# Kernel optimization log

Measured on AMD Instinct MI355X. Metric: run time of the kernel, lower is better.

## Reference

```python
import jax, jax.numpy as jnp
import numpy as np

NUM_SEGMENTS = 64  # number of bags (max batch id + 1)
TEMP = 1.0
EPS_NORM = 1e-12
EPS_SOFTMAX = 1e-16

D = 1024
L = 128
N = 262144


def setup_inputs() -> dict:
    key = jax.random.key(0)
    ks = jax.random.split(key, 8)
    feature = jax.random.normal(ks[0], (N, D), dtype=jnp.float32)
    batch = jnp.sort(jax.random.randint(ks[1], (N,), 0, NUM_SEGMENTS, dtype=jnp.int32))
    # xavier_normal_ init: std = sqrt(2/(fan_in+fan_out))
    Wa = jax.random.normal(ks[2], (L, D), dtype=jnp.float32) * np.sqrt(2.0 / (D + L))
    ba = jnp.zeros((L,), dtype=jnp.float32)
    Wb = jax.random.normal(ks[3], (L, D), dtype=jnp.float32) * np.sqrt(2.0 / (D + L))
    bb = jnp.zeros((L,), dtype=jnp.float32)
    Wc = jax.random.normal(ks[4], (1, L), dtype=jnp.float32) * np.sqrt(2.0 / (L + 1))
    bc = jnp.zeros((1,), dtype=jnp.float32)
    return {"feature": feature, "batch": batch, "istrain": 0,
            "Wa": Wa, "ba": ba, "Wb": Wb, "bb": bb, "Wc": Wc, "bc": bc}


def segment_softmax(score, batch, num_segments):
    # score: [N, 1], batch: [N] segment ids (torch_geometric softmax semantics)
    seg_max = jax.ops.segment_max(score, batch, num_segments=num_segments)
    ex = jnp.exp(score - seg_max[batch])
    denom = jax.ops.segment_sum(ex, batch, num_segments=num_segments)
    return ex / (denom[batch] + EPS_SOFTMAX)


def reference(feature, batch, istrain, Wa, ba, Wb, bb, Wc, bc):
    # F.normalize: L2-normalize each row (dim=1)
    norm = jnp.linalg.norm(feature, axis=1, keepdims=True)
    instance_norm_feature = feature / jnp.maximum(norm, EPS_NORM)
    a = jax.nn.sigmoid(feature @ Wa.T + ba)          # [N, L]
    b = jnp.tanh(feature @ Wb.T + bb)                # [N, L]
    gated = a * b                                     # [N, L]
    score = (gated @ Wc.T + bc) / TEMP               # [N, 1]
    score = segment_softmax(score, batch, NUM_SEGMENTS)
    # istrain=0 -> dropout is identity in this reference
    return (instance_norm_feature, score)
```

## Files before the change

### kernel.cpp

```cpp
#include <hip/hip_runtime.h>

#define DD 1024
#define LL 128
#define NSEG 64
#define CHS 544
#define GRID 1024
#define NT 16

typedef float floatx4 __attribute__((ext_vector_type(4)));

__global__ __launch_bounds__(256)
void prep_kernel(const float* __restrict__ Wa, const float* __restrict__ Wb,
                 unsigned char* __restrict__ Wf8, float* __restrict__ denom,
                 float* __restrict__ score_raw)
{
    int gid = blockIdx.x * 256 + threadIdx.x;
    if (gid < 2 * LL * DD) {
        const int j    = gid & 7;
        const int lane = (gid >> 3) & 63;
        const int ct   = (gid >> 9) & 15;
        const int c    = gid >> 13;
        const int r = ct * 16 + (lane & 15);
        const int k = c * 32 + (lane >> 4) * 8 + j;
        const float v = ((r < LL) ? Wa[r * DD + k] : Wb[(r - LL) * DD + k]) * 16.0f;
        unsigned u = __builtin_amdgcn_cvt_pk_fp8_f32(v, v, 0, false);
        Wf8[gid] = (unsigned char)(u & 0xFF);
        score_raw[gid] = 0.0f;
    }
    if (gid < NSEG) denom[gid] = 0.0f;
}

__global__ __launch_bounds__(512, 8)
void fused_main(const float* __restrict__ feat,
                const unsigned char* __restrict__ Wf8,
                const float* __restrict__ ba,
                const float* __restrict__ bb,
                const float* __restrict__ Wc,
                float* __restrict__ out_norm,
                float* __restrict__ score_raw)
{
    __shared__ __align__(16) char tile[32 * CHS];

    const int tid  = threadIdx.x;
    const int wave = tid >> 6;
    const int lane = tid & 63;
    const int s15  = lane & 15;
    const int l4   = lane >> 4;
    const int bid  = blockIdx.x;

    const float bav = ba[wave * 16 + s15];
    const float bbv = bb[wave * 16 + s15];
    const float wcv = Wc[wave * 16 + s15];
    const unsigned char* bb0 = Wf8 + (size_t)wave * 512 + (size_t)lane * 8;

    float4 L[2][4];

    auto issue = [&](int T) {
        const float* fb = feat + ((size_t)T * 16 + wave * 2) * DD + lane * 4;
        #pragma unroll
        for (int i = 0; i < 2; ++i)
            #pragma unroll
            for (int c = 0; c < 4; ++c)
                L[i][c] = *reinterpret_cast<const float4*>(fb + (size_t)i * DD + c * 256);
    };

    issue(bid);

    for (int it = 0; it < NT; ++it) {
        const int T = bid + it * GRID;

        unsigned pw[2][4];
        #pragma unroll
        for (int i = 0; i < 2; ++i) {
            float ss = 0.0f;
            #pragma unroll
            for (int c = 0; c < 4; ++c)
                ss += L[i][c].x * L[i][c].x + L[i][c].y * L[i][c].y
                    + L[i][c].z * L[i][c].z + L[i][c].w * L[i][c].w;
            #pragma unroll
            for (int off = 32; off >= 1; off >>= 1) ss += __shfl_xor(ss, off);
            const float rinv = 1.0f / fmaxf(sqrtf(ss), 1e-12f);

            float* ob = out_norm + ((size_t)T * 16 + wave * 2 + i) * DD + lane * 4;
            #pragma unroll
            for (int c = 0; c < 4; ++c) {
                float4 v;
                v.x = L[i][c].x * rinv; v.y = L[i][c].y * rinv;
                v.z = L[i][c].z * rinv; v.w = L[i][c].w * rinv;
                *reinterpret_cast<float4*>(ob + c * 256) = v;
            }
            #pragma unroll
            for (int c = 0; c < 4; ++c) {
                unsigned u = __builtin_amdgcn_cvt_pk_fp8_f32(L[i][c].x * 8.0f, L[i][c].y * 8.0f, 0, false);
                u = __builtin_amdgcn_cvt_pk_fp8_f32(L[i][c].z * 8.0f, L[i][c].w * 8.0f, u, true);
                pw[i][c] = u;
            }
        }

        __syncthreads();
        #pragma unroll
        for (int i = 0; i < 2; ++i) {
            const int r = wave * 2 + i;
            #pragma unroll
            for (int c = 0; c < 4; ++c) {
                const int chunk = (lane >> 3) + c * 8;
                const int addr  = chunk * CHS + r * 32 + ((lane >> 1) & 3) * 8 + (lane & 1) * 4;
                *reinterpret_cast<unsigned*>(tile + addr) = pw[i][c];
            }
        }
        __syncthreads();

        if (it + 1 < NT) issue(T + GRID);
        __builtin_amdgcn_sched_barrier(0);

        floatx4 acc0 = (floatx4)0.0f;
        floatx4 acc1 = (floatx4)0.0f;
        #pragma unroll 2
        for (int c = 0; c < 32; ++c) {
            const long long a8 = *reinterpret_cast<const long long*>(tile + c * CHS + s15 * 32 + l4 * 8);
            const long long w0 = *reinterpret_cast<const long long*>(bb0 + (size_t)c * 8192);
            const long long w1 = *reinterpret_cast<const long long*>(bb0 + (size_t)c * 8192 + 4096);
            acc0 = __builtin_amdgcn_mfma_f32_16x16x32_fp8_fp8(a8, w0, acc0, 0, 0, 0);
            acc1 = __builtin_amdgcn_mfma_f32_16x16x32_fp8_fp8(a8, w1, acc1, 0, 0, 0);
        }

        {
            const float S = 1.0f / 128.0f;
            float s[4];
            #pragma unroll
            for (int j = 0; j < 4; ++j) {
                const float av = 1.0f / (1.0f + expf(-(acc0[j] * S + bav)));
                const float bv = tanhf(acc1[j] * S + bbv);
                s[j] = av * bv * wcv;
            }
            #pragma unroll
            for (int j = 0; j < 4; ++j) {
                s[j] += __shfl_xor(s[j], 1);
                s[j] += __shfl_xor(s[j], 2);
                s[j] += __shfl_xor(s[j], 4);
                s[j] += __shfl_xor(s[j], 8);
            }
            if (s15 == 0) {
                #pragma unroll
                for (int j = 0; j < 4; ++j)
                    atomicAdd(&score_raw[(size_t)T * 16 + l4 * 4 + j], s[j]);
            }
        }
    }
}

__global__ __launch_bounds__(256)
void seg_exp_kernel(float* __restrict__ score_inout, const int* __restrict__ batch,
                    float* __restrict__ denom, int n)
{
    __shared__ float sd[NSEG];
    const int t = threadIdx.x;
    if (t < NSEG) sd[t] = 0.0f;
    __syncthreads();
    const int stride = gridDim.x * blockDim.x;
    for (int i = blockIdx.x * blockDim.x + t; i < n; i += stride) {
        const float e = expf(score_inout[i]);
        score_inout[i] = e;
        atomicAdd(&sd[batch[i]], e);
    }
    __syncthreads();
    if (t < NSEG) atomicAdd(&denom[t], sd[t]);
}

__global__ __launch_bounds__(256)
void seg_div_kernel(float* __restrict__ score_inout, const int* __restrict__ batch,
                    const float* __restrict__ denom, int n)
{
    const int stride = gridDim.x * blockDim.x;
    for (int i = blockIdx.x * blockDim.x + threadIdx.x; i < n; i += stride)
        score_inout[i] = score_inout[i] / (denom[batch[i]] + 1e-16f);
}

extern "C" void kernel_launch(void* const* d_in, const int* in_sizes, int n_in,
                              void* d_out, int out_size, void* d_ws, size_t ws_size,
                              hipStream_t stream)
{
    const float* feat  = (const float*)d_in[0];
    const int*   batch = (const int*)d_in[1];
    const float* Wa = (const float*)d_in[3];
    const float* ba = (const float*)d_in[4];
    const float* Wb = (const float*)d_in[5];
    const float* bb = (const float*)d_in[6];
    const float* Wc = (const float*)d_in[7];

    const int N = in_sizes[1];

    float* out_norm  = (float*)d_out;
    float* out_score = (float*)d_out + (size_t)N * DD;

    char* ws = (char*)d_ws;
    unsigned char* Wf8 = (unsigned char*)ws;
    float* denom = (float*)(ws + 2 * LL * DD);

    prep_kernel<<<(2 * LL * DD + 255) / 256, 256, 0, stream>>>(Wa, Wb, Wf8, denom, out_score);
    fused_main<<<GRID, 512, 0, stream>>>(feat, Wf8, ba, bb, Wc, out_norm, out_score);
    seg_exp_kernel<<<512, 256, 0, stream>>>(out_score, batch, denom, N);
    seg_div_kernel<<<512, 256, 0, stream>>>(out_score, batch, denom, N);
}
```

Before: 559.6 us.

## Double-buffer LDS tile and issue next loads before the barrier

The fp8 activation tile in shared memory is now double-buffered by parity, which removes one of the two __syncthreads per tile iteration. The next tile's global loads are issued before the remaining barrier. The grid shrinks to 768 blocks running a grid-stride while-loop, launch bounds drop to 6 waves per SIMD, and the MFMA loop unroll goes from 2 to 4. The aim is to cut barrier stalls and overlap memory with compute, at the cost of twice the LDS per block and a non-uniform tile count per block.

```diff
diff --git a/kernel.cpp b/kernel.cpp
--- a/kernel.cpp
+++ b/kernel.cpp
@@ -4,8 +4,9 @@
 #define LL 128
 #define NSEG 64
 #define CHS 544
-#define GRID 1024
-#define NT 16
+#define TB  17408
+#define GRID 768
+#define NTILE 16384
 
 typedef float floatx4 __attribute__((ext_vector_type(4)));
 
@@ -30,7 +31,7 @@
     if (gid < NSEG) denom[gid] = 0.0f;
 }
 
-__global__ __launch_bounds__(512, 8)
+__global__ __launch_bounds__(512, 6)
 void fused_main(const float* __restrict__ feat,
                 const unsigned char* __restrict__ Wf8,
                 const float* __restrict__ ba,
@@ -39,14 +40,13 @@
                 float* __restrict__ out_norm,
                 float* __restrict__ score_raw)
 {
-    __shared__ __align__(16) char tile[32 * CHS];
+    __shared__ __align__(16) char tile[2 * TB];
 
     const int tid  = threadIdx.x;
     const int wave = tid >> 6;
     const int lane = tid & 63;
     const int s15  = lane & 15;
     const int l4   = lane >> 4;
-    const int bid  = blockIdx.x;
 
     const float bav = ba[wave * 16 + s15];
     const float bbv = bb[wave * 16 + s15];
@@ -55,7 +55,7 @@
 
     float4 L[2][4];
 
-    auto issue = [&](int T) {
+    auto issue = [&](long long T) {
         const float* fb = feat + ((size_t)T * 16 + wave * 2) * DD + lane * 4;
         #pragma unroll
         for (int i = 0; i < 2; ++i)
@@ -64,10 +64,13 @@
                 L[i][c] = *reinterpret_cast<const float4*>(fb + (size_t)i * DD + c * 256);
     };
 
-    issue(bid);
-
-    for (int it = 0; it < NT; ++it) {
-        const int T = bid + it * GRID;
+    long long t = blockIdx.x;
+    int parity = 0;
+    if (t < NTILE) issue(t);
+
+    while (t < NTILE) {
+        const long long row0 = t * 16;
+        char* tb = tile + parity * TB;
 
         unsigned pw[2][4];
         #pragma unroll
@@ -81,7 +84,7 @@
             for (int off = 32; off >= 1; off >>= 1) ss += __shfl_xor(ss, off);
             const float rinv = 1.0f / fmaxf(sqrtf(ss), 1e-12f);
 
-            float* ob = out_norm + ((size_t)T * 16 + wave * 2 + i) * DD + lane * 4;
+            float* ob = out_norm + (row0 + wave * 2 + i) * DD + lane * 4;
             #pragma unroll
             for (int c = 0; c < 4; ++c) {
                 float4 v;
@@ -97,27 +100,28 @@
             }
         }
 
-        __syncthreads();
         #pragma unroll
         for (int i = 0; i < 2; ++i) {
             const int r = wave * 2 + i;
             #pragma unroll
             for (int c = 0; c < 4; ++c) {
                 const int chunk = (lane >> 3) + c * 8;
-                const int addr  = chunk * CHS + r * 32 + ((lane >> 1) & 3) * 8 + (lane & 1) * 4;
+                const int addr  = parity * TB + chunk * CHS + r * 32 + ((lane >> 1) & 3) * 8 + (lane & 1) * 4;
                 *reinterpret_cast<unsigned*>(tile + addr) = pw[i][c];
             }
         }
+
+        const long long tn = t + GRID;
+        if (tn < NTILE) issue(tn);
+        __builtin_amdgcn_sched_barrier(0);
+
         __syncthreads();
-
-        if (it + 1 < NT) issue(T + GRID);
-        __builtin_amdgcn_sched_barrier(0);
 
         floatx4 acc0 = (floatx4)0.0f;
         floatx4 acc1 = (floatx4)0.0f;
-        #pragma unroll 2
+        #pragma unroll 4
         for (int c = 0; c < 32; ++c) {
-            const long long a8 = *reinterpret_cast<const long long*>(tile + c * CHS + s15 * 32 + l4 * 8);
+            const long long a8 = *reinterpret_cast<const long long*>(tb + c * CHS + s15 * 32 + l4 * 8);
             const long long w0 = *reinterpret_cast<const long long*>(bb0 + (size_t)c * 8192);
             const long long w1 = *reinterpret_cast<const long long*>(bb0 + (size_t)c * 8192 + 4096);
             acc0 = __builtin_amdgcn_mfma_f32_16x16x32_fp8_fp8(a8, w0, acc0, 0, 0, 0);
@@ -143,9 +147,12 @@
             if (s15 == 0) {
                 #pragma unroll
                 for (int j = 0; j < 4; ++j)
-                    atomicAdd(&score_raw[(size_t)T * 16 + l4 * 4 + j], s[j]);
-            }
-        }
+                    atomicAdd(&score_raw[row0 + l4 * 4 + j], s[j]);
+            }
+        }
+
+        t = tn;
+        parity ^= 1;
     }
 }
 
```

Measured after the change: 546.4 us. -2.4%, faster.
